# Performance work log

Measured on AMD Instinct MI355X. Metric: run time of the kernel, lower is better.

Reference implementation:

```python
import jax, jax.numpy as jnp
import numpy as np

B, S, D, F, E, K = 64, 512, 512, 2048, 8, 2


def setup_inputs() -> dict:
    key = jax.random.key(0)
    k0, k1, k2, k3 = jax.random.split(key, 4)
    x = jax.random.normal(k0, (B, S, D), dtype=jnp.float32)
    Wr = jax.random.normal(k1, (D, E), dtype=jnp.float32) * (D ** -0.5)
    br = jnp.zeros((E,), dtype=jnp.float32)
    W1 = jax.random.normal(k2, (E, D, F), dtype=jnp.float32) * (D ** -0.5)
    b1 = jnp.zeros((E, F), dtype=jnp.float32)
    W2 = jax.random.normal(k3, (E, F, D), dtype=jnp.float32) * (F ** -0.5)
    b2 = jnp.zeros((E, D), dtype=jnp.float32)
    return {"x": x, "Wr": Wr, "br": br, "W1": W1, "b1": b1, "W2": W2, "b2": b2}


def reference(x, Wr, br, W1, b1, W2, b2):
    orig_shape = x.shape
    t = x.reshape(-1, orig_shape[-1])          # [T, D] flattened tokens
    logits = t @ Wr + br                       # [T, E] router logits
    gates = jax.nn.softmax(logits, axis=-1)
    top_vals, top_idx = jax.lax.top_k(gates, K)      # [T, K]
    top_vals = top_vals / top_vals.sum(axis=-1, keepdims=True)
    # combine weight per (token, expert); zero unless expert is in token's top-k
    onehot = jax.nn.one_hot(top_idx, E, dtype=t.dtype)      # [T, K, E]
    combine = jnp.einsum('tk,tke->te', top_vals, onehot)    # [T, E]
    out = jnp.zeros_like(t)
    for e in range(E):  # small fixed expert count
        h = jax.nn.relu(t @ W1[e] + b1[e])     # [T, F]
        y = h @ W2[e] + b2[e]                  # [T, D]
        out = out + combine[:, e:e + 1] * y
    return out.reshape(orig_shape)
```

## Files before the change

### kernel.cpp

```cpp
#include <hip/hip_runtime.h>

#define T_TOKENS 32768
#define DIM 512
#define FDIM 2048
#define NEXP 8

typedef __attribute__((ext_vector_type(4))) float f32x4;
typedef __attribute__((ext_vector_type(8))) short bf16x8;

__device__ __forceinline__ unsigned short f2bf(float f) {
  unsigned int u = __float_as_uint(f);
  u += 0x7FFFu + ((u >> 16) & 1u);
  return (unsigned short)(u >> 16);
}

#define LGKM_BARRIER()                                        \
  do {                                                        \
    asm volatile("s_waitcnt lgkmcnt(0)" ::: "memory");        \
    __builtin_amdgcn_s_barrier();                             \
  } while (0)

__global__ void pack_w1_kernel(const float* __restrict__ W1, unsigned short* __restrict__ W1p) {
  __shared__ float L[512][17];
  const int b = blockIdx.x;
  const int e = b >> 7, ft = b & 127;
  const int t = threadIdx.x;
  const int c = t & 15, r0 = t >> 4;
  const float* src = W1 + (long)e * 512 * 2048 + ft * 16 + c;
  #pragma unroll
  for (int ch = 0; ch < 32; ch++) {
    int r = ch * 16 + r0;
    L[r][c] = src[(long)r * 2048];
  }
  __syncthreads();
  #pragma unroll
  for (int s = 0; s < 4; s++) {
    int slot = s * 256 + t;
    int kci = slot >> 6, l = slot & 63;
    unsigned short tmp[8];
    #pragma unroll
    for (int j = 0; j < 8; j++)
      tmp[j] = f2bf(L[kci * 32 + (l >> 4) * 8 + j][l & 15]);
    *(ushort4*)(W1p + ((long)b * 16 + kci) * 512 + l * 8)     = *(ushort4*)&tmp[0];
    *(ushort4*)(W1p + ((long)b * 16 + kci) * 512 + l * 8 + 4) = *(ushort4*)&tmp[4];
  }
}

__global__ void pack_w2_kernel(const float* __restrict__ W2, unsigned short* __restrict__ W2p) {
  __shared__ float L[512][17];
  const int b = blockIdx.x;
  const int e = b >> 5, dt = b & 31;
  const int t = threadIdx.x;
  const int c = t & 15, r0 = t >> 4;
  for (int ch = 0; ch < 4; ch++) {
    if (ch) __syncthreads();
    const float* src = W2 + ((long)e * 2048 + ch * 512) * 512 + dt * 16 + c;
    #pragma unroll
    for (int cc = 0; cc < 32; cc++) {
      int r = cc * 16 + r0;
      L[r][c] = src[(long)r * 512];
    }
    __syncthreads();
    #pragma unroll
    for (int s = 0; s < 4; s++) {
      int slot = s * 256 + t;
      int kciL = slot >> 6, l = slot & 63;
      unsigned short tmp[8];
      #pragma unroll
      for (int j = 0; j < 8; j++)
        tmp[j] = f2bf(L[kciL * 32 + (l >> 4) * 8 + j][l & 15]);
      long tt = (long)(e * 64 + ch * 16 + kciL) * 32 + dt;
      *(ushort4*)(W2p + tt * 512 + l * 8)     = *(ushort4*)&tmp[0];
      *(ushort4*)(W2p + tt * 512 + l * 8 + 4) = *(ushort4*)&tmp[4];
    }
  }
}

__global__ void router_kernel(const float* __restrict__ x, const float* __restrict__ Wr,
                              const float* __restrict__ br, int* __restrict__ counts,
                              int* __restrict__ tok_list, float* __restrict__ wt_list,
                              int* __restrict__ slots) {
  __shared__ float WrS[NEXP][DIM];
  __shared__ int lcnt[NEXP];
  __shared__ int lbase[NEXP];
  const int tid = threadIdx.x;
  for (int i = tid; i < NEXP * DIM; i += 256) {
    int e = i >> 9, d = i & (DIM - 1);
    WrS[e][d] = Wr[d * NEXP + e];
  }
  if (tid < NEXP) lcnt[tid] = 0;
  __syncthreads();

  const int t = blockIdx.x * 256 + tid;
  const float* xr = x + (long)t * DIM;
  float acc[NEXP];
  #pragma unroll
  for (int e = 0; e < NEXP; e++) acc[e] = br[e];
  for (int d = 0; d < DIM; d += 4) {
    const float4 xv = *(const float4*)(xr + d);
    #pragma unroll
    for (int e = 0; e < NEXP; e++)
      acc[e] += xv.x * WrS[e][d] + xv.y * WrS[e][d + 1] +
                xv.z * WrS[e][d + 2] + xv.w * WrS[e][d + 3];
  }
  int e0 = 0; float v0 = acc[0];
  #pragma unroll
  for (int e = 1; e < NEXP; e++) if (acc[e] > v0) { v0 = acc[e]; e0 = e; }
  int e1 = -1; float v1 = -3.4e38f;
  #pragma unroll
  for (int e = 0; e < NEXP; e++) if (e != e0 && acc[e] > v1) { v1 = acc[e]; e1 = e; }
  float w0 = 1.f / (1.f + __expf(v1 - v0));
  float w1 = 1.f - w0;

  int l0 = atomicAdd(&lcnt[e0], 1);
  int l1 = atomicAdd(&lcnt[e1], 1);
  __syncthreads();
  if (tid < NEXP) lbase[tid] = atomicAdd(&counts[tid], lcnt[tid]);
  __syncthreads();
  int s0 = lbase[e0] + l0;
  tok_list[e0 * T_TOKENS + s0] = t; wt_list[e0 * T_TOKENS + s0] = w0;
  int s1 = lbase[e1] + l1;
  tok_list[e1 * T_TOKENS + s1] = t; wt_list[e1 * T_TOKENS + s1] = w1;
  if (slots) {
    slots[2 * t]     = e0 * T_TOKENS + s0;
    slots[2 * t + 1] = e1 * T_TOKENS + s1;
  }
}

#define LD_W1(dst, base)                                        \
  _Pragma("unroll")                                             \
  for (int i = 0; i < 4; i++) {                                 \
    dst[i][0] = *(const bf16x8*)(w1b + (base + i) * 512);       \
    dst[i][1] = *(const bf16x8*)(w1b + (16 + base + i) * 512);  \
  }

#define MF_W1(src, base)                                                          \
  _Pragma("unroll")                                                               \
  for (int i = 0; i < 4; i++) {                                                   \
    int kci = base + i;                                                           \
    int xo = ((kci * 4 + g) ^ xsw) << 3;                                          \
    bf16x8 af0 = *(const bf16x8*)&Xs[xbase0 + xo];                                \
    bf16x8 af1 = *(const bf16x8*)&Xs[xbase0 + 16 * 512 + xo];                     \
    H00 = __builtin_amdgcn_mfma_f32_16x16x32_bf16(af0, src[i][0], H00, 0, 0, 0);  \
    H01 = __builtin_amdgcn_mfma_f32_16x16x32_bf16(af0, src[i][1], H01, 0, 0, 0);  \
    H10 = __builtin_amdgcn_mfma_f32_16x16x32_bf16(af1, src[i][0], H10, 0, 0, 0);  \
    H11 = __builtin_amdgcn_mfma_f32_16x16x32_bf16(af1, src[i][1], H11, 0, 0, 0);  \
  }

#define LD_W2(klbase)                                                             \
  _Pragma("unroll")                                                               \
  for (int kl = klbase; kl < klbase + 2; kl++) {                                  \
    const unsigned short* w2b =                                                   \
        W2p + ((long)((e * 64 + (fc >> 5) + kl) * 32 + wave * 4) * 64 + lane) * 8;\
    _Pragma("unroll")                                                             \
    for (int nt = 0; nt < 4; nt++)                                                \
      w2r[kl][nt] = *(const bf16x8*)(w2b + nt * 512);                             \
  }

template <bool USE_PARTIAL>
__global__ __launch_bounds__(512, 2) void ffn_kernel(
    const float* __restrict__ x,
    const unsigned short* __restrict__ W1p,
    const unsigned short* __restrict__ W2p,
    const float* __restrict__ b1, const float* __restrict__ b2,
    const int* __restrict__ counts,
    const int* __restrict__ tok_list, const float* __restrict__ wt_list,
    float* __restrict__ partial,
    float* __restrict__ out) {
  __shared__ unsigned short Xs[64 * 512];
  __shared__ unsigned short Hs[2][64 * 128];

  const int e = blockIdx.x & 7;
  const int tile = blockIdx.x >> 3;
  const int cnt = counts[e];
  const int m0 = tile * 64;
  if (m0 >= cnt) return;
  const int rows = min(64, cnt - m0);

  int pbase = 0;
  if (USE_PARTIAL) {
    #pragma unroll
    for (int i = 0; i < NEXP; i++) pbase += (i < e) ? counts[i] : 0;
  }

  const int tid = threadIdx.x;
  const int wave = tid >> 6, lane = tid & 63;
  const int g = lane >> 4, ln = lane & 15;
  const int mw = wave >> 2, nw = wave & 3;

  #pragma unroll 4
  for (int c = tid; c < 64 * 128; c += 512) {
    int r = c >> 7, q = c & 127;
    ushort4 bv = {0, 0, 0, 0};
    if (r < rows) {
      int tk = tok_list[e * T_TOKENS + m0 + r];
      const f32x4 v = __builtin_nontemporal_load((const f32x4*)(x + (long)tk * DIM + q * 4));
      bv.x = f2bf(v[0]); bv.y = f2bf(v[1]); bv.z = f2bf(v[2]); bv.w = f2bf(v[3]);
    }
    int addr = r * 512 + ((((q >> 1) ^ (r & 7)) << 3) | ((q & 1) << 2));
    *(ushort4*)&Xs[addr] = bv;
  }
  LGKM_BARRIER();

  const f32x4 zero4 = {0.f, 0.f, 0.f, 0.f};
  f32x4 Yacc[4][4];
  #pragma unroll
  for (int a = 0; a < 4; a++)
    #pragma unroll
    for (int b = 0; b < 4; b++) Yacc[a][b] = zero4;

  const int xsw = ln & 7;
  const int xbase0 = (mw * 32 + ln) * 512;

  const unsigned short* const w1b_first =
      W1p + ((long)(e * 128 + nw * 2) * 16) * 512 + lane * 8;
  const unsigned short* w1b = w1b_first;

  bf16x8 wA[4][2], wB[4][2], wC[4][2], w2r[4][4];
  LD_W1(wA, 0);
  LD_W1(wB, 4);

  for (int fc = 0; fc < FDIM; fc += 128) {
    unsigned short* Hp = &Hs[(fc >> 7) & 1][0];
    f32x4 H00 = zero4, H01 = zero4, H10 = zero4, H11 = zero4;

    LD_W1(wC, 8);
    __builtin_amdgcn_s_setprio(1);
    MF_W1(wA, 0);
    MF_W1(wB, 4);
    __builtin_amdgcn_s_setprio(0);
    LD_W1(wB, 12);
    __builtin_amdgcn_s_setprio(1);
    MF_W1(wC, 8);
    __builtin_amdgcn_s_setprio(0);
    LD_W2(0);
    w1b = (fc + 128 < FDIM) ? (w1b + 8 * 16 * 512) : w1b_first;
    LD_W1(wA, 0);
    __builtin_amdgcn_s_setprio(1);
    MF_W1(wB, 12);
    __builtin_amdgcn_s_setprio(0);
    LD_W1(wB, 4);

    {
      float b1v0 = b1[e * FDIM + fc + nw * 32 + ln];
      float b1v1 = b1[e * FDIM + fc + nw * 32 + 16 + ln];
      #pragma unroll
      for (int mi = 0; mi < 2; mi++) {
        #pragma unroll
        for (int ni = 0; ni < 2; ni++) {
          const f32x4& hv = mi ? (ni ? H11 : H10) : (ni ? H01 : H00);
          float bv = ni ? b1v1 : b1v0;
          int fl = nw * 32 + ni * 16 + ln;
          #pragma unroll
          for (int i = 0; i < 4; i++) {
            int m = mw * 32 + mi * 16 + g * 4 + i;
            int addr = m * 128 + ((((fl >> 3) ^ (m & 7)) << 3) | (fl & 7));
            Hp[addr] = f2bf(fmaxf(hv[i] + bv, 0.f));
          }
        }
      }
    }
    LGKM_BARRIER();

    LD_W2(2);

    __builtin_amdgcn_s_setprio(1);
    #pragma unroll
    for (int kl = 0; kl < 4; kl++) {
      bf16x8 ha[4];
      #pragma unroll
      for (int mt = 0; mt < 4; mt++) {
        int m = mt * 16 + ln;
        ha[mt] = *(const bf16x8*)&Hp[m * 128 + ((((kl * 4 + g) ^ (m & 7)) << 3))];
      }
      #pragma unroll
      for (int nt = 0; nt < 4; nt++)
        #pragma unroll
        for (int mt = 0; mt < 4; mt++)
          Yacc[mt][nt] = __builtin_amdgcn_mfma_f32_16x16x32_bf16(ha[mt], w2r[kl][nt], Yacc[mt][nt], 0, 0, 0);
    }
    __builtin_amdgcn_s_setprio(0);
  }

  #pragma unroll
  for (int mt = 0; mt < 4; mt++) {
    #pragma unroll
    for (int i = 0; i < 4; i++) {
      int m = mt * 16 + g * 4 + i;
      if (m < rows) {
        float w = wt_list[e * T_TOKENS + m0 + m];
        if (USE_PARTIAL) {
          float* dst = partial + ((long)(pbase + m0 + m)) * DIM;
          #pragma unroll
          for (int nt = 0; nt < 4; nt++) {
            int d = (wave * 4 + nt) * 16 + ln;
            __builtin_nontemporal_store((Yacc[mt][nt][i] + b2[e * DIM + d]) * w, dst + d);
          }
        } else {
          int tk = tok_list[e * T_TOKENS + m0 + m];
          #pragma unroll
          for (int nt = 0; nt < 4; nt++) {
            int d = (wave * 4 + nt) * 16 + ln;
            float v = (Yacc[mt][nt][i] + b2[e * DIM + d]) * w;
            atomicAdd(out + (long)tk * DIM + d, v);
          }
        }
      }
    }
  }
}

__global__ __launch_bounds__(256) void combine_kernel(
    const float* __restrict__ partial, const int* __restrict__ slots,
    const int* __restrict__ counts, float* __restrict__ out) {
  __shared__ int pre[NEXP];
  if (threadIdx.x == 0) {
    int a = 0;
    #pragma unroll
    for (int i = 0; i < NEXP; i++) { pre[i] = a; a += counts[i]; }
  }
  __syncthreads();
  const int tid = threadIdx.x;
  const int tk = blockIdx.x * 2 + (tid >> 7);
  const int q = (tid & 127) << 2;
  const int2 sp = *(const int2*)(slots + 2 * tk);
  const long r0 = pre[sp.x >> 15] + (sp.x & (T_TOKENS - 1));
  const long r1 = pre[sp.y >> 15] + (sp.y & (T_TOKENS - 1));
  const f32x4 a = __builtin_nontemporal_load((const f32x4*)(partial + r0 * DIM + q));
  const f32x4 b = __builtin_nontemporal_load((const f32x4*)(partial + r1 * DIM + q));
  f32x4 r = a + b;
  __builtin_nontemporal_store(r, (f32x4*)(out + (long)tk * DIM + q));
}

extern "C" void kernel_launch(void* const* d_in, const int* in_sizes, int n_in,
                              void* d_out, int out_size, void* d_ws, size_t ws_size,
                              hipStream_t stream) {
  (void)in_sizes; (void)n_in; (void)out_size;
  const float* x  = (const float*)d_in[0];
  const float* Wr = (const float*)d_in[1];
  const float* br = (const float*)d_in[2];
  const float* W1 = (const float*)d_in[3];
  const float* b1 = (const float*)d_in[4];
  const float* W2 = (const float*)d_in[5];
  const float* b2 = (const float*)d_in[6];
  float* out = (float*)d_out;

  char* ws = (char*)d_ws;
  int*            counts   = (int*)(ws);
  int*            tok_list = (int*)(ws + 1024);
  float*          wt_list  = (float*)(ws + 1049600);
  int*            slots    = (int*)(ws + 2098176);
  unsigned short* W1p      = (unsigned short*)(ws + 2360320);
  unsigned short* W2p      = (unsigned short*)(ws + 19137536);
  float*          partial  = (float*)(ws + 35914752);
  const size_t need_partial = 35914752ull + (size_t)T_TOKENS * 2 * DIM * sizeof(float);
  const bool use_partial = ws_size >= need_partial;

  hipMemsetAsync(counts, 0, 1024, stream);
  pack_w1_kernel<<<NEXP * 128, 256, 0, stream>>>(W1, W1p);
  pack_w2_kernel<<<NEXP * 32, 256, 0, stream>>>(W2, W2p);

  if (use_partial) {
    router_kernel<<<T_TOKENS / 256, 256, 0, stream>>>(x, Wr, br, counts, tok_list, wt_list, slots);
    ffn_kernel<true><<<T_TOKENS / 64 * NEXP, 512, 0, stream>>>(
        x, W1p, W2p, b1, b2, counts, tok_list, wt_list, partial, out);
    combine_kernel<<<T_TOKENS / 2, 256, 0, stream>>>(partial, slots, counts, out);
  } else {
    hipMemsetAsync(out, 0, (size_t)T_TOKENS * DIM * sizeof(float), stream);
    router_kernel<<<T_TOKENS / 256, 256, 0, stream>>>(x, Wr, br, counts, tok_list, wt_list, nullptr);
    ffn_kernel<false><<<T_TOKENS / 64 * NEXP, 512, 0, stream>>>(
        x, W1p, W2p, b1, b2, counts, tok_list, wt_list, nullptr, out);
  }
}
```

Before: 705.6 us.

## Repartition W1 GEMM so each wave owns 16 F-columns across all 64 rows

Changes the first-GEMM wave tiling from a 2x4 (32 rows x 32 F-cols) split to eight waves each computing all 64 token rows for a 16-column F slice. Each wave now loads half as much W1 per chunk, so total W1 global traffic per block drops. In exchange it reads twice as many X fragments from LDS per MFMA. The W1 prefetch also changes from three rotating buffers to two 8-deep buffers, with LD_W2 interleaved between them.

```diff
diff --git a/kernel.cpp b/kernel.cpp
--- a/kernel.cpp
+++ b/kernel.cpp
@@ -127,24 +127,21 @@
   }
 }
 
-#define LD_W1(dst, base)                                        \
+#define LD8(dst, ptr, kbase)                                    \
   _Pragma("unroll")                                             \
-  for (int i = 0; i < 4; i++) {                                 \
-    dst[i][0] = *(const bf16x8*)(w1b + (base + i) * 512);       \
-    dst[i][1] = *(const bf16x8*)(w1b + (16 + base + i) * 512);  \
-  }
-
-#define MF_W1(src, base)                                                          \
-  _Pragma("unroll")                                                               \
-  for (int i = 0; i < 4; i++) {                                                   \
-    int kci = base + i;                                                           \
-    int xo = ((kci * 4 + g) ^ xsw) << 3;                                          \
-    bf16x8 af0 = *(const bf16x8*)&Xs[xbase0 + xo];                                \
-    bf16x8 af1 = *(const bf16x8*)&Xs[xbase0 + 16 * 512 + xo];                     \
-    H00 = __builtin_amdgcn_mfma_f32_16x16x32_bf16(af0, src[i][0], H00, 0, 0, 0);  \
-    H01 = __builtin_amdgcn_mfma_f32_16x16x32_bf16(af0, src[i][1], H01, 0, 0, 0);  \
-    H10 = __builtin_amdgcn_mfma_f32_16x16x32_bf16(af1, src[i][0], H10, 0, 0, 0);  \
-    H11 = __builtin_amdgcn_mfma_f32_16x16x32_bf16(af1, src[i][1], H11, 0, 0, 0);  \
+  for (int i = 0; i < 8; i++)                                   \
+    dst[i] = *(const bf16x8*)((ptr) + (kbase + i) * 512);
+
+#define MF8(src, kbase)                                                            \
+  _Pragma("unroll")                                                                \
+  for (int i = 0; i < 8; i++) {                                                    \
+    int kci = (kbase) + i;                                                         \
+    int xo = ((kci * 4 + g) ^ xsw) << 3;                                           \
+    _Pragma("unroll")                                                              \
+    for (int mt = 0; mt < 4; mt++) {                                               \
+      bf16x8 af = *(const bf16x8*)&Xs[(mt * 16 + ln) * 512 + xo];                  \
+      H[mt] = __builtin_amdgcn_mfma_f32_16x16x32_bf16(af, src[i], H[mt], 0, 0, 0); \
+    }                                                                              \
   }
 
 #define LD_W2(klbase)                                                             \
@@ -186,7 +183,6 @@
   const int tid = threadIdx.x;
   const int wave = tid >> 6, lane = tid & 63;
   const int g = lane >> 4, ln = lane & 15;
-  const int mw = wave >> 2, nw = wave & 3;
 
   #pragma unroll 4
   for (int c = tid; c < 64 * 128; c += 512) {
@@ -210,53 +206,41 @@
     for (int b = 0; b < 4; b++) Yacc[a][b] = zero4;
 
   const int xsw = ln & 7;
-  const int xbase0 = (mw * 32 + ln) * 512;
 
   const unsigned short* const w1b_first =
-      W1p + ((long)(e * 128 + nw * 2) * 16) * 512 + lane * 8;
+      W1p + ((long)(e * 128 + wave) * 16) * 512 + lane * 8;
   const unsigned short* w1b = w1b_first;
 
-  bf16x8 wA[4][2], wB[4][2], wC[4][2], w2r[4][4];
-  LD_W1(wA, 0);
-  LD_W1(wB, 4);
+  bf16x8 wA[8], wB[8], w2r[4][4];
+  LD8(wA, w1b, 0);
 
   for (int fc = 0; fc < FDIM; fc += 128) {
     unsigned short* Hp = &Hs[(fc >> 7) & 1][0];
-    f32x4 H00 = zero4, H01 = zero4, H10 = zero4, H11 = zero4;
-
-    LD_W1(wC, 8);
+    f32x4 H[4];
+    #pragma unroll
+    for (int mt = 0; mt < 4; mt++) H[mt] = zero4;
+
+    LD8(wB, w1b, 8);
     __builtin_amdgcn_s_setprio(1);
-    MF_W1(wA, 0);
-    MF_W1(wB, 4);
-    __builtin_amdgcn_s_setprio(0);
-    LD_W1(wB, 12);
-    __builtin_amdgcn_s_setprio(1);
-    MF_W1(wC, 8);
+    MF8(wA, 0);
     __builtin_amdgcn_s_setprio(0);
     LD_W2(0);
+    __builtin_amdgcn_s_setprio(1);
+    MF8(wB, 8);
+    __builtin_amdgcn_s_setprio(0);
     w1b = (fc + 128 < FDIM) ? (w1b + 8 * 16 * 512) : w1b_first;
-    LD_W1(wA, 0);
-    __builtin_amdgcn_s_setprio(1);
-    MF_W1(wB, 12);
-    __builtin_amdgcn_s_setprio(0);
-    LD_W1(wB, 4);
+    LD8(wA, w1b, 0);
 
     {
-      float b1v0 = b1[e * FDIM + fc + nw * 32 + ln];
-      float b1v1 = b1[e * FDIM + fc + nw * 32 + 16 + ln];
+      float b1v = b1[e * FDIM + fc + wave * 16 + ln];
+      int fl = wave * 16 + ln;
       #pragma unroll
-      for (int mi = 0; mi < 2; mi++) {
+      for (int mt = 0; mt < 4; mt++) {
         #pragma unroll
-        for (int ni = 0; ni < 2; ni++) {
-          const f32x4& hv = mi ? (ni ? H11 : H10) : (ni ? H01 : H00);
-          float bv = ni ? b1v1 : b1v0;
-          int fl = nw * 32 + ni * 16 + ln;
-          #pragma unroll
-          for (int i = 0; i < 4; i++) {
-            int m = mw * 32 + mi * 16 + g * 4 + i;
-            int addr = m * 128 + ((((fl >> 3) ^ (m & 7)) << 3) | (fl & 7));
-            Hp[addr] = f2bf(fmaxf(hv[i] + bv, 0.f));
-          }
+        for (int i = 0; i < 4; i++) {
+          int m = mt * 16 + g * 4 + i;
+          int addr = m * 128 + ((((fl >> 3) ^ (m & 7)) << 3) | (fl & 7));
+          Hp[addr] = f2bf(fmaxf(H[mt][i] + b1v, 0.f));
         }
       }
     }
```

Result: faster. 619.0 us (-12.3%).
